# Kernel optimization log

Hardware: AMD Instinct MI355X
Metric: run time of the kernel (lower is better)

## Reference

```python
import jax, jax.numpy as jnp
from jax import lax
import numpy as np

NUM_KIND = 4
V, H, B = 34, 32, 4096   # raw vertical (2 rows dropped), horizontal, batch
KS = 33                  # odd-rounded max(V-2, H)
NUM_DEPTH = 4
N_SQ = 100


def _conv(x, w):
    # x: (N,1,h,w), w: (1,1,KS,KS); torch Conv2d == cross-correlation == lax default
    return lax.conv_general_dilated(x, w, (1, 1), 'SAME',
                                    dimension_numbers=('NCHW', 'OIHW', 'NCHW'))


def _conv_k(x, w):
    # x: (K,B,1,h,w) -> conv each map with the shared 1-channel kernel
    k, b, c, h, wd = x.shape
    return _conv(x.reshape(k * b, c, h, wd), w).reshape(k, b, c, h, wd)


def setup_inputs() -> dict:
    key = jax.random.key(0)
    ks = jax.random.split(key, 8)
    std = 0.3
    return {
        'dots':    jax.random.randint(ks[0], (V, H, B), 0, NUM_KIND + 1, dtype=jnp.int32),
        'w_each':  jax.random.normal(ks[1], (1, 1, KS, KS), jnp.float32) * std,
        'w_not':   jax.random.normal(ks[2], (1, 1, KS, KS), jnp.float32) * std,
        'w_not2':  jax.random.normal(ks[3], (1, 1, KS, KS), jnp.float32) * std,
        'w_empty': jax.random.normal(ks[4], (1, 1, KS, KS), jnp.float32) * std,
        'W1':      jax.random.normal(ks[5], (N_SQ, (V - 2) * H), jnp.float32) * std,
        'W2':      jax.random.normal(ks[6], (N_SQ, N_SQ), jnp.float32) * std,
        'W3':      jax.random.normal(ks[7], (1, N_SQ), jnp.float32) * std,
    }


def reference(dots, w_each, w_not, w_not2, w_empty, W1, W2, W3):
    # drop last 2 vertical rows, layout (V-2,H,B) -> (B,1,V-2,H)
    board = dots[:-2].astype(jnp.float32).transpose(2, 0, 1)[:, None]  # (B,1,h,w)

    empty = (board == 0).astype(jnp.float32)
    E = _conv(empty, w_empty)                                           # (B,1,h,w)

    kinds = jnp.arange(1, NUM_KIND + 1, dtype=board.dtype).reshape(NUM_KIND, 1, 1, 1, 1)
    each = (board[None] == kinds).astype(jnp.float32)                   # (K,B,1,h,w)
    notm = ((each + empty[None]) == 0).astype(jnp.float32)              # (K,B,1,h,w)

    # first pass: per-color value, masked to that color's cells
    notm_conv = _conv_k(notm, w_not)      # note: the torch code LOGS the convolved not-mask
    v = _conv_k(each, w_each) + E[None] - notm_conv
    L = each * v                          # each_color_value_log (masked)
    s = jax.nn.sigmoid(L.sum(axis=0))     # all_color_value_2nd, (B,1,h,w)

    # iterative diffusion; torch mutates the log in-place each depth:
    # L <- mask * (L + E + conv2nd(notm_conv * before)); before is detached
    for _ in range(NUM_DEPTH):
        before = lax.stop_gradient(s)
        C = _conv_k(notm_conv * before[None], w_not2)
        L = each * (L + E[None] + C)
        s = jax.nn.sigmoid(L.sum(axis=0))

    feat = s.reshape(s.shape[0], -1)      # (B, (V-2)*H)
    x = jax.nn.leaky_relu(feat @ W1.T, 0.2)
    x = jax.nn.leaky_relu(x @ W2.T, 0.2)
    return x @ W3.T                        # (B,1)
```

## Files before the change

kernel.cpp:

```cpp
#include <hip/hip_runtime.h>
#include <cstdint>
#include <cstddef>


typedef _Float16 f16;
typedef __attribute__((ext_vector_type(8))) _Float16 f16x8;
typedef __attribute__((ext_vector_type(4))) float f32x4;

#define NB   4096
#define PIX  1024
#define MR   (NB * 4)

__device__ __forceinline__ void gld_lds16(const void* g, void* l) {
    __builtin_amdgcn_global_load_lds(
        (const __attribute__((address_space(1))) void*)g,
        (__attribute__((address_space(3))) void*)l, 16, 0, 0);
}

__global__ void build_all(const float* __restrict__ we, const float* __restrict__ wn,
                          const float* __restrict__ wn2, const float* __restrict__ wem,
                          const float* __restrict__ W1, const int* __restrict__ dots,
                          f16* __restrict__ Me, f16* __restrict__ Mn,
                          f16* __restrict__ Mn2, f16* __restrict__ Mem,
                          f16* __restrict__ W1b, unsigned char* __restrict__ board) {
    __shared__ unsigned char tile[64][68];
    int bi = blockIdx.x, t = threadIdx.x;
    if (bi < 4096) {
        int idx = bi * 256 + t;
        int o = idx >> 10, in = idx & 1023;
        int i = o >> 5, j = o & 31, a = in >> 5, b = in & 31;
        int u = a - i + 16, v = b - j + 16;
        bool ok = (u >= 0) && (u < 33) && (v >= 0) && (v < 33);
        int w = u * 33 + v;
        float ve = 0.f, vn = 0.f, vn2 = 0.f, vem = 0.f;
        if (ok) { ve = we[w]; vn = wn[w]; vn2 = wn2[w]; vem = wem[w]; }
        Me[idx]  = (f16)ve;
        Mn[idx]  = (f16)vn;
        Mn2[idx] = (f16)vn2;
        Mem[idx] = (f16)vem;
    } else if (bi < 4608) {
        int idx = (bi - 4096) * 256 + t;
        int j = idx >> 10, i = idx & 1023;
        W1b[idx] = (f16)(j < 100 ? W1[j * 1024 + i] : 0.f);
    } else {
        int bb = bi - 4608;
        int bp = bb & 15, bn = bb >> 4;
        int p0 = bp * 64, n0 = bn * 64;
        int ln = t & 63, lp = t >> 6;
#pragma unroll
        for (int j = 0; j < 16; j++) {
            int p = lp * 16 + j;
            tile[p][ln] = (unsigned char)dots[(size_t)(p0 + p) * 4096 + n0 + ln];
        }
        __syncthreads();
#pragma unroll
        for (int j = 0; j < 16; j++) {
            int n = lp * 16 + j;
            board[(size_t)(n0 + n) * 1024 + p0 + ln] = tile[ln][n];
        }
    }
}

template <int MODE, int ASRC>
__device__ __forceinline__ void run_gemm(
    int bjob, int ypx, int nx, char* smem,
    const f16* __restrict__ X, const f16* __restrict__ B,
    const unsigned char* __restrict__ board, const f16* __restrict__ En,
    const f16* __restrict__ NCs, f16* __restrict__ Lsel,
    f16* __restrict__ Pout, f16* __restrict__ outB, int ldo) {
    char* smB = smem;
    char* smA = smem + 16384;

    const int tid = threadIdx.x;
    const int wv = tid >> 6, ln = tid & 63;
    const int wm = wv >> 1, wn_ = wv & 1;
    const int lr = ln & 15, lq = ln >> 4;

    int xcd = bjob & 7, slot = bjob >> 3;
    int bx = slot % nx;
    int by = xcd * ypx + slot / nx;
    const int rtile = by * 128, otile = bx * 128;
    const int img0 = (ASRC == 4) ? rtile : (rtile >> 2);

    const f32x4 fz = {0.f, 0.f, 0.f, 0.f};
    f32x4 acc[4][4];
#pragma unroll
    for (int i = 0; i < 4; i++)
#pragma unroll
        for (int j = 0; j < 4; j++) acc[i][j] = fz;

    for (int kb = 0; kb < 1024; kb += 64) {
#pragma unroll
        for (int t = 0; t < 4; t++) {
            int c = (wv * 4 + t) * 64 + ln;
            int row = c >> 3, gcol = (c & 7) ^ (row & 7);
            gld_lds16(B + (size_t)(otile + row) * 1024 + kb + gcol * 8, smB + c * 16);
        }
        if (ASRC == 0) {
#pragma unroll
            for (int t = 0; t < 4; t++) {
                int c = (wv * 4 + t) * 64 + ln;
                int row = c >> 3, gcol = (c & 7) ^ (row & 7);
                gld_lds16(X + (size_t)(rtile + row) * 1024 + kb + gcol * 8, smA + c * 16);
            }
        } else if (ASRC == 4) {
#pragma unroll
            for (int t = 0; t < 2; t++) {
                int c = t * 256 + wv * 64 + ln;
                int row = c >> 2, g = (c & 3) ^ (row & 3);
                gld_lds16(board + (size_t)(img0 + row) * 1024 + kb + g * 16, smA + c * 16);
            }
        } else {
            if (wv < 2) {
                int c = wv * 64 + ln;
                int row = c >> 2, g = (c & 3) ^ (row & 3);
                gld_lds16(board + (size_t)(img0 + row) * 1024 + kb + g * 16, smA + c * 16);
            }
        }
        __syncthreads();

#pragma unroll
        for (int kk = 0; kk < 2; kk++) {
            const int oct = kk * 4 + lq;
            f16x8 af[4], bfr[4];
#pragma unroll
            for (int i = 0; i < 4; i++) {
                int rrow = wm * 64 + i * 16 + lr;
                if (ASRC == 0) {
                    af[i] = *(const f16x8*)(smA + rrow * 128 + (oct ^ (rrow & 7)) * 16);
                } else {
                    int m = (ASRC == 4) ? rrow : (rrow >> 2);
                    int k1 = (rrow & 3) + 1;
                    uint64_t bb = *(const uint64_t*)(smA + m * 64 +
                                    ((oct >> 1) ^ (m & 3)) * 16 + (oct & 1) * 8);
                    f16x8 v;
#pragma unroll
                    for (int jj = 0; jj < 8; jj++) {
                        int bj = (int)((bb >> (8 * jj)) & 0xff);
                        bool on = (ASRC == 2) ? (bj == k1)
                                : (ASRC == 3) ? (bj != 0 && bj != k1)
                                              : (bj == 0);
                        v[jj] = on ? (f16)1.f : (f16)0.f;
                    }
                    af[i] = v;
                }
            }
#pragma unroll
            for (int j = 0; j < 4; j++) {
                int brow = wn_ * 64 + j * 16 + lr;
                bfr[j] = *(const f16x8*)(smB + brow * 128 + (oct ^ (brow & 7)) * 16);
            }
#pragma unroll
            for (int i = 0; i < 4; i++)
#pragma unroll
                for (int j = 0; j < 4; j++)
                    acc[i][j] = __builtin_amdgcn_mfma_f32_16x16x32_f16(
                        af[i], bfr[j], acc[i][j], 0, 0, 0);
        }
        __syncthreads();
    }

    if constexpr (MODE == 0) {
        f16* sT = (f16*)smem;
#pragma unroll
        for (int i = 0; i < 4; i++) {
            int rb = wm * 64 + i * 16 + lq * 4;
#pragma unroll
            for (int j = 0; j < 4; j++) {
                int col = wn_ * 64 + j * 16 + lr;
                f32x4 a = acc[i][j];
#pragma unroll
                for (int v = 0; v < 4; v++)
                    sT[(rb + v) * 136 + col] = (f16)a[v];
            }
        }
        __syncthreads();
#pragma unroll
        for (int it = 0; it < 8; it++) {
            int row = it * 16 + (tid >> 4), cg = tid & 15;
            f16x8 vv = *(const f16x8*)(sT + row * 136 + cg * 8);
            *(f16x8*)(outB + (size_t)(rtile + row) * ldo + otile + cg * 8) = vv;
        }
    } else {
        float* sAcc = (float*)smem;
#pragma unroll
        for (int h = 0; h < 2; h++) {
            if (wm == h) {
#pragma unroll
                for (int i = 0; i < 4; i++) {
                    int lrow = i * 16 + lq * 4;
#pragma unroll
                    for (int j = 0; j < 4; j++) {
                        int col = wn_ * 64 + j * 16 + lr;
                        f32x4 a = acc[i][j];
#pragma unroll
                        for (int v = 0; v < 4; v++)
                            sAcc[(lrow + v) * 132 + col] = a[v];
                    }
                }
            }
            __syncthreads();
            {
                int cell = tid >> 4, cg = tid & 15;
                int rb = rtile + h * 64 + cell * 4;
                int ngl = rb >> 2;
                int o = otile + cg * 8;
                size_t no = (size_t)ngl * PIX + o;
                uint64_t bb = *(const uint64_t*)(board + no);
                f16x8 en8 = *(const f16x8*)(En + no);
                size_t r0 = (size_t)rb * PIX + o;
                f16x8 nc0 = *(const f16x8*)(NCs + r0);
                f16x8 nc1 = *(const f16x8*)(NCs + r0 + PIX);
                f16x8 nc2 = *(const f16x8*)(NCs + r0 + 2 * PIX);
                f16x8 nc3 = *(const f16x8*)(NCs + r0 + 3 * PIX);
                const float* ar = sAcc + cell * 4 * 132 + cg * 8;
                f32x4 arow[4][2];
#pragma unroll
                for (int k = 0; k < 4; k++) {
                    arow[k][0] = *(const f32x4*)(ar + k * 132);
                    arow[k][1] = *(const f32x4*)(ar + k * 132 + 4);
                }
                f16x8 lout, p0, p1, p2, p3;
#pragma unroll
                for (int j2 = 0; j2 < 8; j2++) {
                    int c = (int)((bb >> (8 * j2)) & 0xff);
                    float a0 = arow[0][j2 >> 2][j2 & 3];
                    float a1 = arow[1][j2 >> 2][j2 & 3];
                    float a2 = arow[2][j2 >> 2][j2 & 3];
                    float a3 = arow[3][j2 >> 2][j2 & 3];
                    float asel = (c == 1) ? a0 : (c == 2) ? a1 : (c == 3) ? a2 : a3;
                    float L = 0.f;
                    if (c > 0) {
                        float ncsel = (float)((c == 1) ? nc0[j2] : (c == 2) ? nc1[j2]
                                            : (c == 3) ? nc2[j2] : nc3[j2]);
                        L = asel + (float)en8[j2] - ncsel;
                    }
                    lout[j2] = (f16)L;
                    f16 s = (f16)(1.f / (1.f + __expf(-L)));
                    p0[j2] = nc0[j2] * s;
                    p1[j2] = nc1[j2] * s;
                    p2[j2] = nc2[j2] * s;
                    p3[j2] = nc3[j2] * s;
                }
                *(f16x8*)(Lsel + no)            = lout;
                *(f16x8*)(Pout + r0)            = p0;
                *(f16x8*)(Pout + r0 + PIX)      = p1;
                *(f16x8*)(Pout + r0 + 2 * PIX)  = p2;
                *(f16x8*)(Pout + r0 + 3 * PIX)  = p3;
            }
            __syncthreads();
        }
    }
}

__global__ void __launch_bounds__(256, 4) gemm_faA(
    const f16* __restrict__ Mn, const f16* __restrict__ Mem,
    const unsigned char* __restrict__ board,
    f16* __restrict__ NC, f16* __restrict__ En) {
    __shared__ __attribute__((aligned(16))) char smem[34816];
    int bi = blockIdx.x;
    if (bi < 1024) {
        run_gemm<0, 3>(bi, 16, 8, smem, nullptr, Mn, board, nullptr, nullptr,
                       nullptr, nullptr, NC, PIX);
    } else {
        run_gemm<0, 4>(bi - 1024, 4, 8, smem, nullptr, Mem, board, nullptr, nullptr,
                       nullptr, nullptr, En, PIX);
    }
}

__global__ void __launch_bounds__(256, 4) gemm_faB(
    const f16* __restrict__ Me, const unsigned char* __restrict__ board,
    const f16* __restrict__ En, const f16* __restrict__ NC,
    f16* __restrict__ Lsel, f16* __restrict__ P1) {
    __shared__ __attribute__((aligned(16))) char smem[36864];
    run_gemm<2, 2>(blockIdx.x, 16, 8, smem, nullptr, Me, board, En, NC,
                   Lsel, P1, nullptr, 0);
}

template <int MODE>
__global__ void __launch_bounds__(256, 2) gemm_depth(
    const f16* __restrict__ Pin, const f16* __restrict__ Mn2,
    const unsigned char* __restrict__ board, const f16* __restrict__ NC,
    const f16* __restrict__ En, f16* __restrict__ Lsel,
    f16* __restrict__ Pout, f16* __restrict__ feat) {
    __shared__ __attribute__((aligned(16))) char smem[36864];
    char* smB = smem;
    char* smA = smem + 16384;

    const int tid = threadIdx.x;
    const int wv = tid >> 6, ln = tid & 63;
    const int wm = wv >> 1, wn_ = wv & 1;
    const int lr = ln & 15, lq = ln >> 4;

    int bi = blockIdx.x;
    int xcd = bi & 7, slot = bi >> 3;
    int bx = slot & 7;
    int by = xcd * 16 + (slot >> 3);
    const int rtile = by * 128, otile = bx * 128;

    const f32x4 fz = {0.f, 0.f, 0.f, 0.f};
    f32x4 acc[4][4];
#pragma unroll
    for (int i = 0; i < 4; i++)
#pragma unroll
        for (int j = 0; j < 4; j++) acc[i][j] = fz;

    for (int kb = 0; kb < 1024; kb += 64) {
#pragma unroll
        for (int t = 0; t < 4; t++) {
            int c = (wv * 4 + t) * 64 + ln;
            int row = c >> 3, gcol = (c & 7) ^ (row & 7);
            gld_lds16(Mn2 + (size_t)(otile + row) * 1024 + kb + gcol * 8, smB + c * 16);
            gld_lds16(Pin + (size_t)(rtile + row) * 1024 + kb + gcol * 8, smA + c * 16);
        }
        __syncthreads();

#pragma unroll
        for (int kk = 0; kk < 2; kk++) {
            const int oct = kk * 4 + lq;
            f16x8 af[4], bfr[4];
#pragma unroll
            for (int i = 0; i < 4; i++) {
                int rrow = wm * 64 + i * 16 + lr;
                af[i] = *(const f16x8*)(smA + rrow * 128 + (oct ^ (rrow & 7)) * 16);
            }
#pragma unroll
            for (int j = 0; j < 4; j++) {
                int brow = wn_ * 64 + j * 16 + lr;
                bfr[j] = *(const f16x8*)(smB + brow * 128 + (oct ^ (brow & 7)) * 16);
            }
#pragma unroll
            for (int i = 0; i < 4; i++)
#pragma unroll
                for (int j = 0; j < 4; j++)
                    acc[i][j] = __builtin_amdgcn_mfma_f32_16x16x32_f16(
                        af[i], bfr[j], acc[i][j], 0, 0, 0);
        }
        __syncthreads();
    }

    float* sAcc = (float*)smem;
#pragma unroll
    for (int h = 0; h < 2; h++) {
        if (wm == h) {
#pragma unroll
            for (int i = 0; i < 4; i++) {
                int lrow = i * 16 + lq * 4;
#pragma unroll
                for (int j = 0; j < 4; j++) {
                    int col = wn_ * 64 + j * 16 + lr;
                    f32x4 a = acc[i][j];
#pragma unroll
                    for (int v = 0; v < 4; v++)
                        sAcc[(lrow + v) * 132 + col] = a[v];
                }
            }
        }
        __syncthreads();
        {
            int cell = tid >> 4, cg = tid & 15;
            int rb = rtile + h * 64 + cell * 4;
            int ngl = rb >> 2;
            int o = otile + cg * 8;
            size_t no = (size_t)ngl * PIX + o;
            uint64_t bb = *(const uint64_t*)(board + no);
            f16x8 en8 = *(const f16x8*)(En + no);
            f16x8 ls8 = *(const f16x8*)(Lsel + no);
            const float* ar = sAcc + cell * 4 * 132 + cg * 8;
            f32x4 arow[4][2];
#pragma unroll
            for (int k = 0; k < 4; k++) {
                arow[k][0] = *(const f32x4*)(ar + k * 132);
                arow[k][1] = *(const f32x4*)(ar + k * 132 + 4);
            }
            if constexpr (MODE == 4) {
                f16x8 s8;
#pragma unroll
                for (int j2 = 0; j2 < 8; j2++) {
                    int c = (int)((bb >> (8 * j2)) & 0xff);
                    float a0 = arow[0][j2 >> 2][j2 & 3];
                    float a1 = arow[1][j2 >> 2][j2 & 3];
                    float a2 = arow[2][j2 >> 2][j2 & 3];
                    float a3 = arow[3][j2 >> 2][j2 & 3];
                    float asel = (c == 1) ? a0 : (c == 2) ? a1 : (c == 3) ? a2 : a3;
                    float L = 0.f;
                    if (c > 0) L = (float)ls8[j2] + (float)en8[j2] + asel;
                    s8[j2] = (f16)(1.f / (1.f + __expf(-L)));
                }
                *(f16x8*)(feat + no) = s8;
            } else {
                size_t r0 = (size_t)rb * PIX + o;
                f16x8 nc0 = *(const f16x8*)(NC + r0);
                f16x8 nc1 = *(const f16x8*)(NC + r0 + PIX);
                f16x8 nc2 = *(const f16x8*)(NC + r0 + 2 * PIX);
                f16x8 nc3 = *(const f16x8*)(NC + r0 + 3 * PIX);
                f16x8 lout, p0, p1, p2, p3;
#pragma unroll
                for (int j2 = 0; j2 < 8; j2++) {
                    int c = (int)((bb >> (8 * j2)) & 0xff);
                    float a0 = arow[0][j2 >> 2][j2 & 3];
                    float a1 = arow[1][j2 >> 2][j2 & 3];
                    float a2 = arow[2][j2 >> 2][j2 & 3];
                    float a3 = arow[3][j2 >> 2][j2 & 3];
                    float asel = (c == 1) ? a0 : (c == 2) ? a1 : (c == 3) ? a2 : a3;
                    float L = 0.f;
                    if (c > 0) L = (float)ls8[j2] + (float)en8[j2] + asel;
                    lout[j2] = (f16)L;
                    f16 s = (f16)(1.f / (1.f + __expf(-L)));
                    p0[j2] = nc0[j2] * s;
                    p1[j2] = nc1[j2] * s;
                    p2[j2] = nc2[j2] * s;
                    p3[j2] = nc3[j2] * s;
                }
                *(f16x8*)(Lsel + no)           = lout;
                *(f16x8*)(Pout + r0)           = p0;
                *(f16x8*)(Pout + r0 + PIX)     = p1;
                *(f16x8*)(Pout + r0 + 2 * PIX) = p2;
                *(f16x8*)(Pout + r0 + 3 * PIX) = p3;
            }
        }
        __syncthreads();
    }
}

__global__ void __launch_bounds__(256) gemm_mlp_fused(
    const f16* __restrict__ feat, const f16* __restrict__ W1b,
    const float* __restrict__ W2, const float* __restrict__ W3,
    float* __restrict__ out) {
    __shared__ __attribute__((aligned(16))) char smem[47360];
    char* smB = smem;
    char* smA = smem + 16384;

    const int tid = threadIdx.x;
    const int wv = tid >> 6, ln = tid & 63;
    const int wm = wv >> 1, wn_ = wv & 1;
    const int lr = ln & 15, lq = ln >> 4;
    const int rtile = blockIdx.x * 128;

    const f32x4 fz = {0.f, 0.f, 0.f, 0.f};
    f32x4 acc[4][4];
#pragma unroll
    for (int i = 0; i < 4; i++)
#pragma unroll
        for (int j = 0; j < 4; j++) acc[i][j] = fz;

    for (int kb = 0; kb < 1024; kb += 64) {
#pragma unroll
        for (int t = 0; t < 4; t++) {
            int c = (wv * 4 + t) * 64 + ln;
            int row = c >> 3, gcol = (c & 7) ^ (row & 7);
            gld_lds16(W1b  + (size_t)row * 1024 + kb + gcol * 8, smB + c * 16);
            gld_lds16(feat + (size_t)(rtile + row) * 1024 + kb + gcol * 8, smA + c * 16);
        }
        __syncthreads();
#pragma unroll
        for (int kk = 0; kk < 2; kk++) {
            const int oct = kk * 4 + lq;
            f16x8 af[4], bfr[4];
#pragma unroll
            for (int i = 0; i < 4; i++) {
                int rrow = wm * 64 + i * 16 + lr;
                af[i] = *(const f16x8*)(smA + rrow * 128 + (oct ^ (rrow & 7)) * 16);
            }
#pragma unroll
            for (int j = 0; j < 4; j++) {
                int brow = wn_ * 64 + j * 16 + lr;
                bfr[j] = *(const f16x8*)(smB + brow * 128 + (oct ^ (brow & 7)) * 16);
            }
#pragma unroll
            for (int i = 0; i < 4; i++)
#pragma unroll
                for (int j = 0; j < 4; j++)
                    acc[i][j] = __builtin_amdgcn_mfma_f32_16x16x32_f16(
                        af[i], bfr[j], acc[i][j], 0, 0, 0);
        }
        __syncthreads();
    }

    float* xs  = (float*)smem;
    f16*   sW2 = (f16*)(smem + 25856);
    float* sW3 = (float*)(smem + 45856);
    float* red = (float*)(smem + 46272);
    for (int idx = tid; idx < 10000; idx += 256) sW2[idx] = (f16)W2[idx];
    if (tid < 100) sW3[tid] = W3[tid];

    for (int half = 0; half < 2; half++) {
        if (wm == half) {
#pragma unroll
            for (int i = 0; i < 4; i++) {
                int rb = i * 16 + lq * 4;
#pragma unroll
                for (int j = 0; j < 4; j++) {
                    int o = wn_ * 64 + j * 16 + lr;
                    if (o < 100) {
                        f32x4 a = acc[i][j];
#pragma unroll
                        for (int v = 0; v < 4; v++) {
                            float x = a[v];
                            xs[(rb + v) * 101 + o] = x > 0.f ? x : 0.2f * x;
                        }
                    }
                }
            }
        }
        __syncthreads();
        int nb = tid >> 2, q = tid & 3;
        const float* xrow = xs + nb * 101;
        float partial = 0.f;
        for (int jj = 0; jj < 25; jj++) {
            int j = q + jj * 4;
            const f16* w2r = sW2 + j * 100;
            float a2 = 0.f;
#pragma unroll
            for (int i = 0; i < 100; i++) a2 += (float)w2r[i] * xrow[i];
            partial += sW3[j] * (a2 > 0.f ? a2 : 0.2f * a2);
        }
        red[tid] = partial;
        __syncthreads();
        if (q == 0)
            out[rtile + half * 64 + nb] = red[tid] + red[tid + 1] + red[tid + 2] + red[tid + 3];
        __syncthreads();
    }
}

extern "C" void kernel_launch(void* const* d_in, const int* in_sizes, int n_in,
                              void* d_out, int out_size, void* d_ws, size_t ws_size,
                              hipStream_t stream) {
    (void)in_sizes; (void)n_in; (void)out_size; (void)ws_size;
    const int*   dots   = (const int*)d_in[0];
    const float* w_each = (const float*)d_in[1];
    const float* w_not  = (const float*)d_in[2];
    const float* w_not2 = (const float*)d_in[3];
    const float* w_emp  = (const float*)d_in[4];
    const float* W1 = (const float*)d_in[5];
    const float* W2 = (const float*)d_in[6];
    const float* W3 = (const float*)d_in[7];
    float* out = (float*)d_out;

    char* ws = (char*)d_ws;
    size_t off = 0;
    auto alloc = [&](size_t bytes) -> char* {
        char* p = ws + off;
        off += (bytes + 255) & ~(size_t)255;
        return p;
    };
    f16* Me    = (f16*)alloc((size_t)PIX * PIX * 2);
    f16* Mn    = (f16*)alloc((size_t)PIX * PIX * 2);
    f16* Mn2   = (f16*)alloc((size_t)PIX * PIX * 2);
    f16* Mem   = (f16*)alloc((size_t)PIX * PIX * 2);
    f16* W1b   = (f16*)alloc((size_t)128 * PIX * 2);
    unsigned char* board = (unsigned char*)alloc((size_t)NB * PIX);
    f16* NC    = (f16*)alloc((size_t)MR * PIX * 2);
    f16* En    = (f16*)alloc((size_t)NB * PIX * 2);
    f16* Pa    = (f16*)alloc((size_t)MR * PIX * 2);
    f16* Pb    = (f16*)alloc((size_t)MR * PIX * 2);
    f16* feat  = (f16*)alloc((size_t)NB * PIX * 2);
    f16* Lsel  = (f16*)alloc((size_t)NB * PIX * 2);

    dim3 blk(256);
    build_all<<<5632, blk, 0, stream>>>(w_each, w_not, w_not2, w_emp, W1, dots,
                                        Me, Mn, Mn2, Mem, W1b, board);
    gemm_faA<<<1280, blk, 0, stream>>>(Mn, Mem, board, NC, En);
    gemm_faB<<<1024, blk, 0, stream>>>(Me, board, En, NC, Lsel, Pa);
    gemm_depth<3><<<1024, blk, 0, stream>>>(Pa, Mn2, board, NC, En, Lsel, Pb, nullptr);
    gemm_depth<3><<<1024, blk, 0, stream>>>(Pb, Mn2, board, NC, En, Lsel, Pa, nullptr);
    gemm_depth<3><<<1024, blk, 0, stream>>>(Pa, Mn2, board, NC, En, Lsel, Pb, nullptr);
    gemm_depth<4><<<1024, blk, 0, stream>>>(Pb, Mn2, board, NC, En, Lsel, nullptr, feat);
    gemm_mlp_fused<<<32, blk, 0, stream>>>(feat, W1b, W2, W3, out);
}
```

Before: 416.4 us.

## Precompute f16 color masks in a separate kernel instead of decoding in GEMM loops

```diff
diff --git a/kernel.cpp b/kernel.cpp
--- a/kernel.cpp
+++ b/kernel.cpp
@@ -61,7 +61,37 @@
     }
 }
 
-template <int MODE, int ASRC>
+__global__ void expand_masks(const unsigned char* __restrict__ board,
+                             f16* __restrict__ eachF, f16* __restrict__ notmF,
+                             f16* __restrict__ emptyF) {
+    int bi = blockIdx.x, t = threadIdx.x;
+    if (bi < 8192) {
+        int idx = bi * 256 + t;
+        int r = idx >> 7, w0 = (idx & 127) << 3;
+        int n = r >> 2, k1 = (r & 3) + 1;
+        uint64_t bb = *(const uint64_t*)(board + (size_t)n * 1024 + w0);
+        f16x8 e, m;
+#pragma unroll
+        for (int j = 0; j < 8; j++) {
+            int bj = (int)((bb >> (8 * j)) & 0xff);
+            e[j] = (bj == k1) ? (f16)1.f : (f16)0.f;
+            m[j] = (bj != 0 && bj != k1) ? (f16)1.f : (f16)0.f;
+        }
+        *(f16x8*)(eachF + (size_t)idx * 8) = e;
+        *(f16x8*)(notmF + (size_t)idx * 8) = m;
+    } else {
+        int idx = (bi - 8192) * 256 + t;
+        int n = idx >> 7, w0 = (idx & 127) << 3;
+        uint64_t bb = *(const uint64_t*)(board + (size_t)n * 1024 + w0);
+        f16x8 e;
+#pragma unroll
+        for (int j = 0; j < 8; j++)
+            e[j] = (((bb >> (8 * j)) & 0xff) == 0) ? (f16)1.f : (f16)0.f;
+        *(f16x8*)(emptyF + (size_t)idx * 8) = e;
+    }
+}
+
+template <int MODE>
 __device__ __forceinline__ void run_gemm(
     int bjob, int ypx, int nx, char* smem,
     const f16* __restrict__ X, const f16* __restrict__ B,
@@ -80,7 +110,6 @@
     int bx = slot % nx;
     int by = xcd * ypx + slot / nx;
     const int rtile = by * 128, otile = bx * 128;
-    const int img0 = (ASRC == 4) ? rtile : (rtile >> 2);
 
     const f32x4 fz = {0.f, 0.f, 0.f, 0.f};
     f32x4 acc[4][4];
@@ -95,27 +124,7 @@
             int c = (wv * 4 + t) * 64 + ln;
             int row = c >> 3, gcol = (c & 7) ^ (row & 7);
             gld_lds16(B + (size_t)(otile + row) * 1024 + kb + gcol * 8, smB + c * 16);
-        }
-        if (ASRC == 0) {
-#pragma unroll
-            for (int t = 0; t < 4; t++) {
-                int c = (wv * 4 + t) * 64 + ln;
-                int row = c >> 3, gcol = (c & 7) ^ (row & 7);
-                gld_lds16(X + (size_t)(rtile + row) * 1024 + kb + gcol * 8, smA + c * 16);
-            }
-        } else if (ASRC == 4) {
-#pragma unroll
-            for (int t = 0; t < 2; t++) {
-                int c = t * 256 + wv * 64 + ln;
-                int row = c >> 2, g = (c & 3) ^ (row & 3);
-                gld_lds16(board + (size_t)(img0 + row) * 1024 + kb + g * 16, smA + c * 16);
-            }
-        } else {
-            if (wv < 2) {
-                int c = wv * 64 + ln;
-                int row = c >> 2, g = (c & 3) ^ (row & 3);
-                gld_lds16(board + (size_t)(img0 + row) * 1024 + kb + g * 16, smA + c * 16);
-            }
+            gld_lds16(X + (size_t)(rtile + row) * 1024 + kb + gcol * 8, smA + c * 16);
         }
         __syncthreads();
 
@@ -126,24 +135,7 @@
 #pragma unroll
             for (int i = 0; i < 4; i++) {
                 int rrow = wm * 64 + i * 16 + lr;
-                if (ASRC == 0) {
-                    af[i] = *(const f16x8*)(smA + rrow * 128 + (oct ^ (rrow & 7)) * 16);
-                } else {
-                    int m = (ASRC == 4) ? rrow : (rrow >> 2);
-                    int k1 = (rrow & 3) + 1;
-                    uint64_t bb = *(const uint64_t*)(smA + m * 64 +
-                                    ((oct >> 1) ^ (m & 3)) * 16 + (oct & 1) * 8);
-                    f16x8 v;
-#pragma unroll
-                    for (int jj = 0; jj < 8; jj++) {
-                        int bj = (int)((bb >> (8 * jj)) & 0xff);
-                        bool on = (ASRC == 2) ? (bj == k1)
-                                : (ASRC == 3) ? (bj != 0 && bj != k1)
-                                              : (bj == 0);
-                        v[jj] = on ? (f16)1.f : (f16)0.f;
-                    }
-                    af[i] = v;
-                }
+                af[i] = *(const f16x8*)(smA + rrow * 128 + (oct ^ (rrow & 7)) * 16);
             }
 #pragma unroll
             for (int j = 0; j < 4; j++) {
@@ -255,30 +247,30 @@
 
 __global__ void __launch_bounds__(256, 4) gemm_faA(
     const f16* __restrict__ Mn, const f16* __restrict__ Mem,
-    const unsigned char* __restrict__ board,
+    const f16* __restrict__ notmF, const f16* __restrict__ emptyF,
     f16* __restrict__ NC, f16* __restrict__ En) {
     __shared__ __attribute__((aligned(16))) char smem[34816];
     int bi = blockIdx.x;
     if (bi < 1024) {
-        run_gemm<0, 3>(bi, 16, 8, smem, nullptr, Mn, board, nullptr, nullptr,
-                       nullptr, nullptr, NC, PIX);
+        run_gemm<0>(bi, 16, 8, smem, notmF, Mn, nullptr, nullptr, nullptr,
+                    nullptr, nullptr, NC, PIX);
     } else {
-        run_gemm<0, 4>(bi - 1024, 4, 8, smem, nullptr, Mem, board, nullptr, nullptr,
-                       nullptr, nullptr, En, PIX);
+        run_gemm<0>(bi - 1024, 4, 8, smem, emptyF, Mem, nullptr, nullptr, nullptr,
+                    nullptr, nullptr, En, PIX);
     }
 }
 
 __global__ void __launch_bounds__(256, 4) gemm_faB(
-    const f16* __restrict__ Me, const unsigned char* __restrict__ board,
-    const f16* __restrict__ En, const f16* __restrict__ NC,
-    f16* __restrict__ Lsel, f16* __restrict__ P1) {
+    const f16* __restrict__ Me, const f16* __restrict__ eachF,
+    const unsigned char* __restrict__ board, const f16* __restrict__ En,
+    const f16* __restrict__ NC, f16* __restrict__ Lsel, f16* __restrict__ P1) {
     __shared__ __attribute__((aligned(16))) char smem[36864];
-    run_gemm<2, 2>(blockIdx.x, 16, 8, smem, nullptr, Me, board, En, NC,
-                   Lsel, P1, nullptr, 0);
+    run_gemm<2>(blockIdx.x, 16, 8, smem, eachF, Me, board, En, NC,
+                Lsel, P1, nullptr, 0);
 }
 
 template <int MODE>
-__global__ void __launch_bounds__(256, 2) gemm_depth(
+__global__ void __launch_bounds__(256, 4) gemm_depth(
     const f16* __restrict__ Pin, const f16* __restrict__ Mn2,
     const unsigned char* __restrict__ board, const f16* __restrict__ NC,
     const f16* __restrict__ En, f16* __restrict__ Lsel,
@@ -550,18 +542,22 @@
     f16* Mem   = (f16*)alloc((size_t)PIX * PIX * 2);
     f16* W1b   = (f16*)alloc((size_t)128 * PIX * 2);
     unsigned char* board = (unsigned char*)alloc((size_t)NB * PIX);
+    f16* eachF = (f16*)alloc((size_t)MR * PIX * 2);
+    f16* notmF = (f16*)alloc((size_t)MR * PIX * 2);
+    f16* emptyF= (f16*)alloc((size_t)NB * PIX * 2);
     f16* NC    = (f16*)alloc((size_t)MR * PIX * 2);
     f16* En    = (f16*)alloc((size_t)NB * PIX * 2);
-    f16* Pa    = (f16*)alloc((size_t)MR * PIX * 2);
-    f16* Pb    = (f16*)alloc((size_t)MR * PIX * 2);
+    f16* Lsel  = (f16*)alloc((size_t)NB * PIX * 2);
     f16* feat  = (f16*)alloc((size_t)NB * PIX * 2);
-    f16* Lsel  = (f16*)alloc((size_t)NB * PIX * 2);
+    f16* Pa = notmF;
+    f16* Pb = eachF;
 
     dim3 blk(256);
     build_all<<<5632, blk, 0, stream>>>(w_each, w_not, w_not2, w_emp, W1, dots,
                                         Me, Mn, Mn2, Mem, W1b, board);
-    gemm_faA<<<1280, blk, 0, stream>>>(Mn, Mem, board, NC, En);
-    gemm_faB<<<1024, blk, 0, stream>>>(Me, board, En, NC, Lsel, Pa);
+    expand_masks<<<10240, blk, 0, stream>>>(board, eachF, notmF, emptyF);
+    gemm_faA<<<1280, blk, 0, stream>>>(Mn, Mem, notmF, emptyF, NC, En);
+    gemm_faB<<<1024, blk, 0, stream>>>(Me, eachF, board, En, NC, Lsel, Pa);
     gemm_depth<3><<<1024, blk, 0, stream>>>(Pa, Mn2, board, NC, En, Lsel, Pb, nullptr);
     gemm_depth<3><<<1024, blk, 0, stream>>>(Pb, Mn2, board, NC, En, Lsel, Pa, nullptr);
     gemm_depth<3><<<1024, blk, 0, stream>>>(Pa, Mn2, board, NC, En, Lsel, Pb, nullptr);
```

Result: faster. 391.2 us (-6.1%).
